# Performance work log

Measured on AMD Instinct MI355X. Metric: run time of the kernel, lower is better.

Reference implementation:

```python
import jax, jax.numpy as jnp
import numpy as np

K = 2  # top-k experts kept


def setup_inputs() -> dict:
    key = jax.random.key(0)
    k1, k2, k3 = jax.random.split(key, 3)
    M, B, D, H = 8, 8192, 1024, 256
    zs = jax.random.normal(k1, (M, B, D), dtype=jnp.float32)
    W1 = jax.random.normal(k2, (M * D, H), dtype=jnp.float32) * 0.02
    b1 = jnp.zeros((H,), dtype=jnp.float32)
    W2 = jax.random.normal(k3, (H, M), dtype=jnp.float32) * 0.02
    b2 = jnp.zeros((M,), dtype=jnp.float32)
    return {"zs": zs, "W1": W1, "b1": b1, "W2": W2, "b2": b2}


def reference(zs, W1, b1, W2, b2):
    M, B, D = zs.shape
    # torch.cat(zs, dim=-1) -> [B, M*D]
    cat = jnp.transpose(zs, (1, 0, 2)).reshape(B, M * D)
    # gate MLP: Linear -> GELU(exact) -> Linear
    h = jax.nn.gelu(cat @ W1 + b1, approximate=False)
    logits = h @ W2 + b2                      # [B, M]
    # eval path: no noise added
    topk_logits, topk_idx = jax.lax.top_k(logits, K)  # [B, K]
    topk_w = jax.nn.softmax(topk_logits, axis=-1)     # [B, K]
    # scatter top-k weights into dense [B, M] routing matrix
    rows = jnp.arange(B)[:, None]
    w = jnp.zeros_like(logits).at[rows, topk_idx].set(topk_w)
    # fused = sum_i zs[i] * w[:, i:i+1]
    fused = jnp.einsum("mbd,bm->bd", zs, w)
    return fused, w
```

## Files before the change

kernel.cpp:

```cpp
#include <hip/hip_runtime.h>
#include <math.h>

constexpr int B_ = 8192;
constexpr int D_ = 1024;
constexpr int M_ = 8;
constexpr int H_ = 256;
constexpr int SPLITK = 4;
constexpr int KSP = 2048;
constexpr int BM = 128, BN = 256, BK = 16;
constexpr int NCH = KSP / BK;

typedef __bf16 bf16x8 __attribute__((ext_vector_type(8)));
typedef float  f32x16 __attribute__((ext_vector_type(16)));
typedef short  short8 __attribute__((ext_vector_type(8)));

__device__ __forceinline__ unsigned short f2bf(float x) {
    unsigned int u = __float_as_uint(x);
    u += 0x7FFFu + ((u >> 16) & 1u);
    return (unsigned short)(u >> 16);
}
__device__ __forceinline__ float bf2f(unsigned short s) {
    return __uint_as_float(((unsigned int)s) << 16);
}

#define MFMA(A, Bf, C) __builtin_amdgcn_mfma_f32_32x32x16_bf16((A), (Bf), (C), 0, 0, 0)

__global__ __launch_bounds__(256, 1)
void gemm1_kernel(const float* __restrict__ zs, const float* __restrict__ W1,
                  float* __restrict__ part)
{
    __shared__ short Ah[2 * 128 * 8], Am_[2 * 128 * 8], Al[2 * 128 * 8];
    __shared__ short Bh[2 * 256 * 8], Bm_[2 * 256 * 8], Bl[2 * 256 * 8];

    const int t  = threadIdx.x;
    const int b0 = blockIdx.x * BM;
    const int s  = blockIdx.y;
    const int k0 = s * KSP;

    const int amr = t >> 1;
    const int aks = t & 1;

    const int lane = t & 63;
    const int wv   = t >> 6;
    const int kl   = lane >> 5;
    const int ln   = lane & 31;

    f32x16 acc[8];
#pragma unroll
    for (int i = 0; i < 8; ++i) acc[i] = (f32x16)0.0f;

    float4 a0, a1;
    float  bv[16];

#define LOAD_REGS(KG) {                                                        \
    const int kgv = (KG);                                                      \
    const float* pz = zs + ((size_t)(kgv >> 10) * B_ + b0 + amr) * D_          \
                         + (kgv & 1023) + aks * 8;                             \
    a0 = *(const float4*)pz;                                                   \
    a1 = *(const float4*)(pz + 4);                                             \
    const float* pw = W1 + (size_t)kgv * H_ + t;                               \
    _Pragma("unroll")                                                          \
    for (int k2 = 0; k2 < 16; ++k2) bv[k2] = pw[k2 * H_];                      \
}

#define SPLIT_STORE() {                                                        \
    float av[8] = {a0.x, a0.y, a0.z, a0.w, a1.x, a1.y, a1.z, a1.w};            \
    short8 vh, vm, vl;                                                         \
    _Pragma("unroll")                                                          \
    for (int j = 0; j < 8; ++j) {                                              \
        unsigned short h = f2bf(av[j]);                                        \
        float r = av[j] - bf2f(h);                                             \
        unsigned short mm = f2bf(r);                                           \
        r = r - bf2f(mm);                                                      \
        unsigned short ll = f2bf(r);                                           \
        vh[j] = (short)h; vm[j] = (short)mm; vl[j] = (short)ll;                \
    }                                                                          \
    const int ia = aks * 128 + (amr ^ aks);                                    \
    *(short8*)&Ah[ia * 8]  = vh;                                               \
    *(short8*)&Am_[ia * 8] = vm;                                               \
    *(short8*)&Al[ia * 8]  = vl;                                               \
    _Pragma("unroll")                                                          \
    for (int ks = 0; ks < 2; ++ks) {                                           \
        short8 wh, wm, wl;                                                     \
        _Pragma("unroll")                                                      \
        for (int j = 0; j < 8; ++j) {                                          \
            unsigned short h = f2bf(bv[ks * 8 + j]);                           \
            float r = bv[ks * 8 + j] - bf2f(h);                                \
            unsigned short mm = f2bf(r);                                       \
            r = r - bf2f(mm);                                                  \
            unsigned short ll = f2bf(r);                                       \
            wh[j] = (short)h; wm[j] = (short)mm; wl[j] = (short)ll;            \
        }                                                                      \
        const int ib = ks * 256 + t;                                           \
        *(short8*)&Bh[ib * 8]  = wh;                                           \
        *(short8*)&Bm_[ib * 8] = wm;                                           \
        *(short8*)&Bl[ib * 8]  = wl;                                           \
    }                                                                          \
}

    LOAD_REGS(k0)
    SPLIT_STORE()
    __syncthreads();

#pragma unroll 1
    for (int c = 0; c < NCH; ++c) {
        if (c + 1 < NCH) LOAD_REGS(k0 + (c + 1) * BK)

        {
            const int ib0 = kl * 256 + wv * 64 + ln;
            const bf16x8 bh0 = __builtin_bit_cast(bf16x8, *(const short8*)&Bh[ib0 * 8]);
            const bf16x8 bm0 = __builtin_bit_cast(bf16x8, *(const short8*)&Bm_[ib0 * 8]);
            const bf16x8 bl0 = __builtin_bit_cast(bf16x8, *(const short8*)&Bl[ib0 * 8]);
            const bf16x8 bh1 = __builtin_bit_cast(bf16x8, *(const short8*)&Bh[(ib0 + 32) * 8]);
            const bf16x8 bm1 = __builtin_bit_cast(bf16x8, *(const short8*)&Bm_[(ib0 + 32) * 8]);
            const bf16x8 bl1 = __builtin_bit_cast(bf16x8, *(const short8*)&Bl[(ib0 + 32) * 8]);
#pragma unroll
            for (int rt = 0; rt < 4; ++rt) {
                const int ia = kl * 128 + ((rt * 32 + ln) ^ kl);
                const bf16x8 ah = __builtin_bit_cast(bf16x8, *(const short8*)&Ah[ia * 8]);
                const bf16x8 aM = __builtin_bit_cast(bf16x8, *(const short8*)&Am_[ia * 8]);
                const bf16x8 aL = __builtin_bit_cast(bf16x8, *(const short8*)&Al[ia * 8]);
                acc[rt*2+0] = MFMA(ah, bh0, acc[rt*2+0]);
                acc[rt*2+0] = MFMA(ah, bm0, acc[rt*2+0]);
                acc[rt*2+0] = MFMA(aM, bh0, acc[rt*2+0]);
                acc[rt*2+0] = MFMA(aM, bm0, acc[rt*2+0]);
                acc[rt*2+0] = MFMA(ah, bl0, acc[rt*2+0]);
                acc[rt*2+0] = MFMA(aL, bh0, acc[rt*2+0]);
                acc[rt*2+1] = MFMA(ah, bh1, acc[rt*2+1]);
                acc[rt*2+1] = MFMA(ah, bm1, acc[rt*2+1]);
                acc[rt*2+1] = MFMA(aM, bh1, acc[rt*2+1]);
                acc[rt*2+1] = MFMA(aM, bm1, acc[rt*2+1]);
                acc[rt*2+1] = MFMA(ah, bl1, acc[rt*2+1]);
                acc[rt*2+1] = MFMA(aL, bh1, acc[rt*2+1]);
            }
        }

        if (c + 1 < NCH) {
            __syncthreads();
            SPLIT_STORE()
            __syncthreads();
        }
    }
#undef LOAD_REGS
#undef SPLIT_STORE

    float* P = part + ((size_t)s * B_ + b0) * H_;
#pragma unroll
    for (int rt = 0; rt < 4; ++rt) {
#pragma unroll
        for (int ctl = 0; ctl < 2; ++ctl) {
            const f32x16 v = acc[rt * 2 + ctl];
            const int col = wv * 64 + ctl * 32 + ln;
#pragma unroll
            for (int r = 0; r < 16; ++r) {
                const int row = rt * 32 + (r & 3) + 8 * (r >> 2) + 4 * kl;
                P[(size_t)row * H_ + col] = v[r];
            }
        }
    }
}

__device__ __forceinline__ float gelu_exact(float x) {
    return 0.5f * x * (1.0f + erff(x * 0.70710678118654752f));
}

__global__ __launch_bounds__(256)
void gate_kernel(const float* __restrict__ part, const float* __restrict__ b1,
                 const float* __restrict__ W2, const float* __restrict__ b2,
                 float* __restrict__ w_out, int2* __restrict__ sel,
                 float2* __restrict__ wt)
{
    const int t    = threadIdx.x;
    const int wv   = t >> 6;
    const int lane = t & 63;
    const int row  = blockIdx.x * 4 + wv;

    const float* pr = part + (size_t)row * H_ + lane * 4;
    float4 x = *(const float4*)pr;
    const float4 x1 = *(const float4*)(pr + (size_t)B_ * H_);
    const float4 x2 = *(const float4*)(pr + (size_t)2 * B_ * H_);
    const float4 x3 = *(const float4*)(pr + (size_t)3 * B_ * H_);
    const float4 bb = *(const float4*)&b1[lane * 4];
    const float h0 = gelu_exact(x.x + x1.x + x2.x + x3.x + bb.x);
    const float h1 = gelu_exact(x.y + x1.y + x2.y + x3.y + bb.y);
    const float h2 = gelu_exact(x.z + x1.z + x2.z + x3.z + bb.z);
    const float h3 = gelu_exact(x.w + x1.w + x2.w + x3.w + bb.w);

    float lg[8] = {0, 0, 0, 0, 0, 0, 0, 0};
    const int cb = lane * 4;
#define ACC8(HC, CI) {                                                         \
    const float4 wa_ = *(const float4*)&W2[(cb + (CI)) * 8];                   \
    const float4 wb_ = *(const float4*)&W2[(cb + (CI)) * 8 + 4];               \
    lg[0] = fmaf((HC), wa_.x, lg[0]); lg[1] = fmaf((HC), wa_.y, lg[1]);        \
    lg[2] = fmaf((HC), wa_.z, lg[2]); lg[3] = fmaf((HC), wa_.w, lg[3]);        \
    lg[4] = fmaf((HC), wb_.x, lg[4]); lg[5] = fmaf((HC), wb_.y, lg[5]);        \
    lg[6] = fmaf((HC), wb_.z, lg[6]); lg[7] = fmaf((HC), wb_.w, lg[7]);        \
}
    ACC8(h0, 0) ACC8(h1, 1) ACC8(h2, 2) ACC8(h3, 3)
#undef ACC8

#pragma unroll
    for (int off = 32; off >= 1; off >>= 1) {
#pragma unroll
        for (int i = 0; i < 8; ++i) lg[i] += __shfl_xor(lg[i], off, 64);
    }

    if (lane == 0) {
        float l[8];
#pragma unroll
        for (int i = 0; i < 8; ++i) l[i] = lg[i] + b2[i];
        int i1 = 0; float l1 = l[0];
#pragma unroll
        for (int i = 1; i < 8; ++i) if (l[i] > l1) { l1 = l[i]; i1 = i; }
        int i2 = (i1 == 0) ? 1 : 0; float l2 = l[i2];
#pragma unroll
        for (int i = 0; i < 8; ++i)
            if (i != i1 && l[i] > l2) { l2 = l[i]; i2 = i; }

        const float e  = expf(l2 - l1);
        const float dn = 1.0f + e;
        const float wa = 1.0f / dn;
        const float wb = e / dn;

        float* wr = w_out + (size_t)row * M_;
#pragma unroll
        for (int i = 0; i < 8; ++i)
            wr[i] = (i == i1) ? wa : ((i == i2) ? wb : 0.0f);
        sel[row] = make_int2(i1, i2);
        wt[row]  = make_float2(wa, wb);
    }
}

__global__ __launch_bounds__(256)
void combine_kernel(const float* __restrict__ zs, const int2* __restrict__ sel,
                    const float2* __restrict__ wt, float* __restrict__ fused)
{
    const int b = blockIdx.x;
    const int2   e = sel[b];
    const float2 w = wt[b];
    const float4* z1 = (const float4*)(zs + ((size_t)e.x * B_ + b) * D_);
    const float4* z2 = (const float4*)(zs + ((size_t)e.y * B_ + b) * D_);
    float4* o = (float4*)(fused + (size_t)b * D_);
    const int d = threadIdx.x;
    const float4 x = z1[d];
    const float4 y = z2[d];
    o[d] = make_float4(fmaf(w.x, x.x, w.y * y.x),
                       fmaf(w.x, x.y, w.y * y.y),
                       fmaf(w.x, x.z, w.y * y.z),
                       fmaf(w.x, x.w, w.y * y.w));
}

extern "C" void kernel_launch(void* const* d_in, const int* in_sizes, int n_in,
                              void* d_out, int out_size, void* d_ws, size_t ws_size,
                              hipStream_t stream)
{
    const float* zs = (const float*)d_in[0];
    const float* W1 = (const float*)d_in[1];
    const float* b1 = (const float*)d_in[2];
    const float* W2 = (const float*)d_in[3];
    const float* b2 = (const float*)d_in[4];

    float* fused = (float*)d_out;
    float* w_out = fused + (size_t)B_ * D_;

    float*  part = (float*)d_ws;
    int2*   sel  = (int2*)(part + (size_t)SPLITK * B_ * H_);
    float2* wt   = (float2*)(sel + B_);

    gemm1_kernel<<<dim3(B_ / BM, SPLITK), 256, 0, stream>>>(zs, W1, part);
    gate_kernel<<<dim3(B_ / 4), 256, 0, stream>>>(part, b1, W2, b2, w_out, sel, wt);
    combine_kernel<<<dim3(B_), 256, 0, stream>>>(zs, sel, wt, fused);
}
```

Baseline: 545.4 us.

## Pre-split W1 into bf16 triples, stage B via direct LDS loads, fuse gate+combine

```diff
diff --git a/kernel.cpp b/kernel.cpp
--- a/kernel.cpp
+++ b/kernel.cpp
@@ -5,14 +5,17 @@
 constexpr int D_ = 1024;
 constexpr int M_ = 8;
 constexpr int H_ = 256;
+
 constexpr int SPLITK = 4;
 constexpr int KSP = 2048;
-constexpr int BM = 128, BN = 256, BK = 16;
+constexpr int BM = 64, BK = 16;
 constexpr int NCH = KSP / BK;
+constexpr int NG  = (M_ * D_) / BK;
 
 typedef __bf16 bf16x8 __attribute__((ext_vector_type(8)));
 typedef float  f32x16 __attribute__((ext_vector_type(16)));
 typedef short  short8 __attribute__((ext_vector_type(8)));
+typedef short  short4v __attribute__((ext_vector_type(4)));
 
 __device__ __forceinline__ unsigned short f2bf(float x) {
     unsigned int u = __float_as_uint(x);
@@ -25,128 +28,154 @@
 
 #define MFMA(A, Bf, C) __builtin_amdgcn_mfma_f32_32x32x16_bf16((A), (Bf), (C), 0, 0, 0)
 
-__global__ __launch_bounds__(256, 1)
-void gemm1_kernel(const float* __restrict__ zs, const float* __restrict__ W1,
+#define GLOAD_LDS16(gp, lp)                                                    \
+    __builtin_amdgcn_global_load_lds(                                          \
+        (const __attribute__((address_space(1))) void*)(gp),                   \
+        (__attribute__((address_space(3))) void*)(lp), 16, 0, 0)
+
+__global__ __launch_bounds__(256)
+void splitw1_kernel(const float* __restrict__ W1, short* __restrict__ Ph,
+                    short* __restrict__ Pm, short* __restrict__ Pl)
+{
+    const int g = blockIdx.x;
+    const int t = threadIdx.x;
+    float v[16];
+#pragma unroll
+    for (int k = 0; k < 16; ++k) v[k] = W1[(size_t)(g * 16 + k) * H_ + t];
+#pragma unroll
+    for (int ks = 0; ks < 2; ++ks) {
+        short8 vh, vm, vl;
+#pragma unroll
+        for (int j = 0; j < 8; ++j) {
+            const float x = v[ks * 8 + j];
+            const unsigned short h = f2bf(x);
+            float r = x - bf2f(h);
+            const unsigned short m = f2bf(r);
+            r = r - bf2f(m);
+            const unsigned short l = f2bf(r);
+            vh[j] = (short)h; vm[j] = (short)m; vl[j] = (short)l;
+        }
+        const size_t o = ((size_t)(g * 2 + ks) * 256 + t) * 8;
+        *(short8*)&Ph[o] = vh;
+        *(short8*)&Pm[o] = vm;
+        *(short8*)&Pl[o] = vl;
+    }
+}
+
+__global__ __launch_bounds__(256, 2)
+void gemm1_kernel(const float* __restrict__ zs,
+                  const short* __restrict__ Ph,
+                  const short* __restrict__ Pm,
+                  const short* __restrict__ Pl,
                   float* __restrict__ part)
 {
-    __shared__ short Ah[2 * 128 * 8], Am_[2 * 128 * 8], Al[2 * 128 * 8];
-    __shared__ short Bh[2 * 256 * 8], Bm_[2 * 256 * 8], Bl[2 * 256 * 8];
+    __shared__ short Ah[2][1024], Am_[2][1024], Al[2][1024];
+    __shared__ short Bh[2][4096], Bm_[2][4096], Bl[2][4096];
 
     const int t  = threadIdx.x;
     const int b0 = blockIdx.x * BM;
-    const int s  = blockIdx.y;
-    const int k0 = s * KSP;
-
-    const int amr = t >> 1;
-    const int aks = t & 1;
+    const int g0 = blockIdx.y * NCH;
+
+    const int ar  = t >> 2;
+    const int ap  = t & 3;
+    const int aof = ((ap >> 1) * 64 + ar) * 8 + (ap & 1) * 4;
 
     const int lane = t & 63;
     const int wv   = t >> 6;
     const int kl   = lane >> 5;
     const int ln   = lane & 31;
 
-    f32x16 acc[8];
-#pragma unroll
-    for (int i = 0; i < 8; ++i) acc[i] = (f32x16)0.0f;
-
-    float4 a0, a1;
-    float  bv[16];
-
-#define LOAD_REGS(KG) {                                                        \
-    const int kgv = (KG);                                                      \
-    const float* pz = zs + ((size_t)(kgv >> 10) * B_ + b0 + amr) * D_          \
-                         + (kgv & 1023) + aks * 8;                             \
-    a0 = *(const float4*)pz;                                                   \
-    a1 = *(const float4*)(pz + 4);                                             \
-    const float* pw = W1 + (size_t)kgv * H_ + t;                               \
-    _Pragma("unroll")                                                          \
-    for (int k2 = 0; k2 < 16; ++k2) bv[k2] = pw[k2 * H_];                      \
-}
-
-#define SPLIT_STORE() {                                                        \
-    float av[8] = {a0.x, a0.y, a0.z, a0.w, a1.x, a1.y, a1.z, a1.w};            \
-    short8 vh, vm, vl;                                                         \
-    _Pragma("unroll")                                                          \
-    for (int j = 0; j < 8; ++j) {                                              \
-        unsigned short h = f2bf(av[j]);                                        \
-        float r = av[j] - bf2f(h);                                             \
-        unsigned short mm = f2bf(r);                                           \
-        r = r - bf2f(mm);                                                      \
-        unsigned short ll = f2bf(r);                                           \
-        vh[j] = (short)h; vm[j] = (short)mm; vl[j] = (short)ll;                \
-    }                                                                          \
-    const int ia = aks * 128 + (amr ^ aks);                                    \
-    *(short8*)&Ah[ia * 8]  = vh;                                               \
-    *(short8*)&Am_[ia * 8] = vm;                                               \
-    *(short8*)&Al[ia * 8]  = vl;                                               \
+    f32x16 acc[4];
+#pragma unroll
+    for (int i = 0; i < 4; ++i) acc[i] = (f32x16)0.0f;
+
+    float4 areg;
+
+#define STAGE_B(BUF, G) {                                                      \
     _Pragma("unroll")                                                          \
     for (int ks = 0; ks < 2; ++ks) {                                           \
-        short8 wh, wm, wl;                                                     \
-        _Pragma("unroll")                                                      \
-        for (int j = 0; j < 8; ++j) {                                          \
-            unsigned short h = f2bf(bv[ks * 8 + j]);                           \
-            float r = bv[ks * 8 + j] - bf2f(h);                                \
-            unsigned short mm = f2bf(r);                                       \
-            r = r - bf2f(mm);                                                  \
-            unsigned short ll = f2bf(r);                                       \
-            wh[j] = (short)h; wm[j] = (short)mm; wl[j] = (short)ll;            \
-        }                                                                      \
-        const int ib = ks * 256 + t;                                           \
-        *(short8*)&Bh[ib * 8]  = wh;                                           \
-        *(short8*)&Bm_[ib * 8] = wm;                                           \
-        *(short8*)&Bl[ib * 8]  = wl;                                           \
+        const size_t so = (((size_t)(G) * 2 + ks) * 256 + t) * 8;              \
+        const int   dof = (ks * 256 + t) * 8;                                  \
+        GLOAD_LDS16(Ph + so, &Bh[BUF][dof]);                                   \
+        GLOAD_LDS16(Pm + so, &Bm_[BUF][dof]);                                  \
+        GLOAD_LDS16(Pl + so, &Bl[BUF][dof]);                                   \
     }                                                                          \
 }
 
-    LOAD_REGS(k0)
-    SPLIT_STORE()
+#define LOAD_A(G) {                                                            \
+    const int kg = (G) * 16;                                                   \
+    areg = *(const float4*)(zs + ((size_t)(kg >> 10) * B_ + b0 + ar) * D_      \
+                               + (kg & 1023) + ap * 4);                        \
+}
+
+#define STORE_A(BUF) {                                                         \
+    const float av[4] = {areg.x, areg.y, areg.z, areg.w};                      \
+    short4v vh, vm, vl;                                                        \
+    _Pragma("unroll")                                                          \
+    for (int j = 0; j < 4; ++j) {                                              \
+        const unsigned short h = f2bf(av[j]);                                  \
+        float r = av[j] - bf2f(h);                                             \
+        const unsigned short m = f2bf(r);                                      \
+        r = r - bf2f(m);                                                       \
+        const unsigned short l = f2bf(r);                                      \
+        vh[j] = (short)h; vm[j] = (short)m; vl[j] = (short)l;                  \
+    }                                                                          \
+    *(short4v*)&Ah[BUF][aof]  = vh;                                            \
+    *(short4v*)&Am_[BUF][aof] = vm;                                            \
+    *(short4v*)&Al[BUF][aof]  = vl;                                            \
+}
+
+    STAGE_B(0, g0)
+    LOAD_A(g0)
+    STORE_A(0)
     __syncthreads();
 
+    int buf = 0;
 #pragma unroll 1
     for (int c = 0; c < NCH; ++c) {
-        if (c + 1 < NCH) LOAD_REGS(k0 + (c + 1) * BK)
-
+        if (c + 1 < NCH) {
+            STAGE_B(buf ^ 1, g0 + c + 1)
+            LOAD_A(g0 + c + 1)
+        }
         {
-            const int ib0 = kl * 256 + wv * 64 + ln;
-            const bf16x8 bh0 = __builtin_bit_cast(bf16x8, *(const short8*)&Bh[ib0 * 8]);
-            const bf16x8 bm0 = __builtin_bit_cast(bf16x8, *(const short8*)&Bm_[ib0 * 8]);
-            const bf16x8 bl0 = __builtin_bit_cast(bf16x8, *(const short8*)&Bl[ib0 * 8]);
-            const bf16x8 bh1 = __builtin_bit_cast(bf16x8, *(const short8*)&Bh[(ib0 + 32) * 8]);
-            const bf16x8 bm1 = __builtin_bit_cast(bf16x8, *(const short8*)&Bm_[(ib0 + 32) * 8]);
-            const bf16x8 bl1 = __builtin_bit_cast(bf16x8, *(const short8*)&Bl[(ib0 + 32) * 8]);
-#pragma unroll
-            for (int rt = 0; rt < 4; ++rt) {
-                const int ia = kl * 128 + ((rt * 32 + ln) ^ kl);
-                const bf16x8 ah = __builtin_bit_cast(bf16x8, *(const short8*)&Ah[ia * 8]);
-                const bf16x8 aM = __builtin_bit_cast(bf16x8, *(const short8*)&Am_[ia * 8]);
-                const bf16x8 aL = __builtin_bit_cast(bf16x8, *(const short8*)&Al[ia * 8]);
-                acc[rt*2+0] = MFMA(ah, bh0, acc[rt*2+0]);
-                acc[rt*2+0] = MFMA(ah, bm0, acc[rt*2+0]);
-                acc[rt*2+0] = MFMA(aM, bh0, acc[rt*2+0]);
-                acc[rt*2+0] = MFMA(aM, bm0, acc[rt*2+0]);
-                acc[rt*2+0] = MFMA(ah, bl0, acc[rt*2+0]);
-                acc[rt*2+0] = MFMA(aL, bh0, acc[rt*2+0]);
-                acc[rt*2+1] = MFMA(ah, bh1, acc[rt*2+1]);
-                acc[rt*2+1] = MFMA(ah, bm1, acc[rt*2+1]);
-                acc[rt*2+1] = MFMA(aM, bh1, acc[rt*2+1]);
-                acc[rt*2+1] = MFMA(aM, bm1, acc[rt*2+1]);
-                acc[rt*2+1] = MFMA(ah, bl1, acc[rt*2+1]);
-                acc[rt*2+1] = MFMA(aL, bh1, acc[rt*2+1]);
-            }
-        }
-
-        if (c + 1 < NCH) {
-            __syncthreads();
-            SPLIT_STORE()
-            __syncthreads();
-        }
-    }
-#undef LOAD_REGS
-#undef SPLIT_STORE
-
-    float* P = part + ((size_t)s * B_ + b0) * H_;
-#pragma unroll
-    for (int rt = 0; rt < 4; ++rt) {
+            const int ib = (kl * 256 + wv * 64 + ln) * 8;
+            const bf16x8 bh0 = __builtin_bit_cast(bf16x8, *(const short8*)&Bh[buf][ib]);
+            const bf16x8 bm0 = __builtin_bit_cast(bf16x8, *(const short8*)&Bm_[buf][ib]);
+            const bf16x8 bl0 = __builtin_bit_cast(bf16x8, *(const short8*)&Bl[buf][ib]);
+            const bf16x8 bh1 = __builtin_bit_cast(bf16x8, *(const short8*)&Bh[buf][ib + 256]);
+            const bf16x8 bm1 = __builtin_bit_cast(bf16x8, *(const short8*)&Bm_[buf][ib + 256]);
+            const bf16x8 bl1 = __builtin_bit_cast(bf16x8, *(const short8*)&Bl[buf][ib + 256]);
+            const int ia = (kl * 64 + ln) * 8;
+            const bf16x8 ah0 = __builtin_bit_cast(bf16x8, *(const short8*)&Ah[buf][ia]);
+            const bf16x8 am0 = __builtin_bit_cast(bf16x8, *(const short8*)&Am_[buf][ia]);
+            const bf16x8 al0 = __builtin_bit_cast(bf16x8, *(const short8*)&Al[buf][ia]);
+            const bf16x8 ah1 = __builtin_bit_cast(bf16x8, *(const short8*)&Ah[buf][ia + 256]);
+            const bf16x8 am1 = __builtin_bit_cast(bf16x8, *(const short8*)&Am_[buf][ia + 256]);
+            const bf16x8 al1 = __builtin_bit_cast(bf16x8, *(const short8*)&Al[buf][ia + 256]);
+            acc[0] = MFMA(ah0, bh0, acc[0]); acc[1] = MFMA(ah0, bh1, acc[1]);
+            acc[2] = MFMA(ah1, bh0, acc[2]); acc[3] = MFMA(ah1, bh1, acc[3]);
+            acc[0] = MFMA(ah0, bm0, acc[0]); acc[1] = MFMA(ah0, bm1, acc[1]);
+            acc[2] = MFMA(ah1, bm0, acc[2]); acc[3] = MFMA(ah1, bm1, acc[3]);
+            acc[0] = MFMA(am0, bh0, acc[0]); acc[1] = MFMA(am0, bh1, acc[1]);
+            acc[2] = MFMA(am1, bh0, acc[2]); acc[3] = MFMA(am1, bh1, acc[3]);
+            acc[0] = MFMA(am0, bm0, acc[0]); acc[1] = MFMA(am0, bm1, acc[1]);
+            acc[2] = MFMA(am1, bm0, acc[2]); acc[3] = MFMA(am1, bm1, acc[3]);
+            acc[0] = MFMA(ah0, bl0, acc[0]); acc[1] = MFMA(ah0, bl1, acc[1]);
+            acc[2] = MFMA(ah1, bl0, acc[2]); acc[3] = MFMA(ah1, bl1, acc[3]);
+            acc[0] = MFMA(al0, bh0, acc[0]); acc[1] = MFMA(al0, bh1, acc[1]);
+            acc[2] = MFMA(al1, bh0, acc[2]); acc[3] = MFMA(al1, bh1, acc[3]);
+        }
+        if (c + 1 < NCH) STORE_A(buf ^ 1)
+        __syncthreads();
+        buf ^= 1;
+    }
+#undef STAGE_B
+#undef LOAD_A
+#undef STORE_A
+
+    float* P = part + ((size_t)blockIdx.y * B_ + b0) * H_;
+#pragma unroll
+    for (int rt = 0; rt < 2; ++rt) {
 #pragma unroll
         for (int ctl = 0; ctl < 2; ++ctl) {
             const f32x16 v = acc[rt * 2 + ctl];
@@ -165,10 +194,10 @@
 }
 
 __global__ __launch_bounds__(256)
-void gate_kernel(const float* __restrict__ part, const float* __restrict__ b1,
-                 const float* __restrict__ W2, const float* __restrict__ b2,
-                 float* __restrict__ w_out, int2* __restrict__ sel,
-                 float2* __restrict__ wt)
+void gate_combine_kernel(const float* __restrict__ part, const float* __restrict__ b1,
+                         const float* __restrict__ W2, const float* __restrict__ b2,
+                         const float* __restrict__ zs, float* __restrict__ fused,
+                         float* __restrict__ w_out)
 {
     const int t    = threadIdx.x;
     const int wv   = t >> 6;
@@ -176,15 +205,15 @@
     const int row  = blockIdx.x * 4 + wv;
 
     const float* pr = part + (size_t)row * H_ + lane * 4;
-    float4 x = *(const float4*)pr;
+    const float4 x0 = *(const float4*)pr;
     const float4 x1 = *(const float4*)(pr + (size_t)B_ * H_);
     const float4 x2 = *(const float4*)(pr + (size_t)2 * B_ * H_);
     const float4 x3 = *(const float4*)(pr + (size_t)3 * B_ * H_);
     const float4 bb = *(const float4*)&b1[lane * 4];
-    const float h0 = gelu_exact(x.x + x1.x + x2.x + x3.x + bb.x);
-    const float h1 = gelu_exact(x.y + x1.y + x2.y + x3.y + bb.y);
-    const float h2 = gelu_exact(x.z + x1.z + x2.z + x3.z + bb.z);
-    const float h3 = gelu_exact(x.w + x1.w + x2.w + x3.w + bb.w);
+    const float h0 = gelu_exact(x0.x + x1.x + x2.x + x3.x + bb.x);
+    const float h1 = gelu_exact(x0.y + x1.y + x2.y + x3.y + bb.y);
+    const float h2 = gelu_exact(x0.z + x1.z + x2.z + x3.z + bb.z);
+    const float h3 = gelu_exact(x0.w + x1.w + x2.w + x3.w + bb.w);
 
     float lg[8] = {0, 0, 0, 0, 0, 0, 0, 0};
     const int cb = lane * 4;
@@ -205,49 +234,42 @@
         for (int i = 0; i < 8; ++i) lg[i] += __shfl_xor(lg[i], off, 64);
     }
 
+    float l[8];
+#pragma unroll
+    for (int i = 0; i < 8; ++i) l[i] = lg[i] + b2[i];
+    int i1 = 0; float l1 = l[0];
+#pragma unroll
+    for (int i = 1; i < 8; ++i) if (l[i] > l1) { l1 = l[i]; i1 = i; }
+    int i2 = (i1 == 0) ? 1 : 0; float l2 = l[i2];
+#pragma unroll
+    for (int i = 0; i < 8; ++i)
+        if (i != i1 && l[i] > l2) { l2 = l[i]; i2 = i; }
+
+    const float e  = expf(l2 - l1);
+    const float dn = 1.0f + e;
+    const float wa = 1.0f / dn;
+    const float wb = e / dn;
+
     if (lane == 0) {
-        float l[8];
-#pragma unroll
-        for (int i = 0; i < 8; ++i) l[i] = lg[i] + b2[i];
-        int i1 = 0; float l1 = l[0];
-#pragma unroll
-        for (int i = 1; i < 8; ++i) if (l[i] > l1) { l1 = l[i]; i1 = i; }
-        int i2 = (i1 == 0) ? 1 : 0; float l2 = l[i2];
-#pragma unroll
-        for (int i = 0; i < 8; ++i)
-            if (i != i1 && l[i] > l2) { l2 = l[i]; i2 = i; }
-
-        const float e  = expf(l2 - l1);
-        const float dn = 1.0f + e;
-        const float wa = 1.0f / dn;
-        const float wb = e / dn;
-
         float* wr = w_out + (size_t)row * M_;
 #pragma unroll
         for (int i = 0; i < 8; ++i)
             wr[i] = (i == i1) ? wa : ((i == i2) ? wb : 0.0f);
-        sel[row] = make_int2(i1, i2);
-        wt[row]  = make_float2(wa, wb);
-    }
-}
-
-__global__ __launch_bounds__(256)
-void combine_kernel(const float* __restrict__ zs, const int2* __restrict__ sel,
-                    const float2* __restrict__ wt, float* __restrict__ fused)
-{
-    const int b = blockIdx.x;
-    const int2   e = sel[b];
-    const float2 w = wt[b];
-    const float4* z1 = (const float4*)(zs + ((size_t)e.x * B_ + b) * D_);
-    const float4* z2 = (const float4*)(zs + ((size_t)e.y * B_ + b) * D_);
-    float4* o = (float4*)(fused + (size_t)b * D_);
-    const int d = threadIdx.x;
-    const float4 x = z1[d];
-    const float4 y = z2[d];
-    o[d] = make_float4(fmaf(w.x, x.x, w.y * y.x),
-                       fmaf(w.x, x.y, w.y * y.y),
-                       fmaf(w.x, x.z, w.y * y.z),
-                       fmaf(w.x, x.w, w.y * y.w));
+    }
+
+    const float4* z1 = (const float4*)(zs + ((size_t)i1 * B_ + row) * D_);
+    const float4* z2 = (const float4*)(zs + ((size_t)i2 * B_ + row) * D_);
+    float4* o = (float4*)(fused + (size_t)row * D_);
+#pragma unroll
+    for (int i = 0; i < 4; ++i) {
+        const int d = lane + i * 64;
+        const float4 x = z1[d];
+        const float4 y = z2[d];
+        o[d] = make_float4(fmaf(wa, x.x, wb * y.x),
+                           fmaf(wa, x.y, wb * y.y),
+                           fmaf(wa, x.z, wb * y.z),
+                           fmaf(wa, x.w, wb * y.w));
+    }
 }
 
 extern "C" void kernel_launch(void* const* d_in, const int* in_sizes, int n_in,
@@ -263,11 +285,13 @@
     float* fused = (float*)d_out;
     float* w_out = fused + (size_t)B_ * D_;
 
-    float*  part = (float*)d_ws;
-    int2*   sel  = (int2*)(part + (size_t)SPLITK * B_ * H_);
-    float2* wt   = (float2*)(sel + B_);
-
-    gemm1_kernel<<<dim3(B_ / BM, SPLITK), 256, 0, stream>>>(zs, W1, part);
-    gate_kernel<<<dim3(B_ / 4), 256, 0, stream>>>(part, b1, W2, b2, w_out, sel, wt);
-    combine_kernel<<<dim3(B_), 256, 0, stream>>>(zs, sel, wt, fused);
-}
+    float* part = (float*)d_ws;
+    short* Ph = (short*)(part + (size_t)SPLITK * B_ * H_);
+    const size_t PSZ = (size_t)NG * 2 * 256 * 8;
+    short* Pm = Ph + PSZ;
+    short* Pl = Pm + PSZ;
+
+    splitw1_kernel<<<NG, 256, 0, stream>>>(W1, Ph, Pm, Pl);
+    gemm1_kernel<<<dim3(B_ / BM, SPLITK), 256, 0, stream>>>(zs, Ph, Pm, Pl, part);
+    gate_combine_kernel<<<dim3(B_ / 4), 256, 0, stream>>>(part, b1, W2, b2, zs, fused, w_out);
+}
```

Result: faster. 528.7 us (-3.1%).
